# Optimization experiments

Measured on AMD Instinct MI355X. Metric: run time of the kernel, lower is better.

Reference implementation:

```python
import jax, jax.numpy as jnp
import numpy as np

D_MODEL = 1024
D_HEAD = 64
B, S = 4, 2048


def setup_inputs() -> dict:
    key = jax.random.key(0)
    ks = jax.random.split(key, 4)
    scale = 1.0 / np.sqrt(D_MODEL)
    return {
        "embeddings": jax.random.normal(ks[0], (B, S, D_MODEL), dtype=jnp.float32),
        "Wq": jax.random.normal(ks[1], (D_MODEL, D_HEAD), dtype=jnp.float32) * scale,
        "bq": jnp.zeros((D_HEAD,), dtype=jnp.float32),
        "Wk": jax.random.normal(ks[2], (D_MODEL, D_HEAD), dtype=jnp.float32) * scale,
        "bk": jnp.zeros((D_HEAD,), dtype=jnp.float32),
        "Wv": jax.random.normal(ks[3], (D_MODEL, D_HEAD), dtype=jnp.float32) * scale,
        "bv": jnp.zeros((D_HEAD,), dtype=jnp.float32),
    }


def reference(embeddings, Wq, bq, Wk, bk, Wv, bv):
    # Q, K, V projections: (b, s, d_head)
    Q = embeddings @ Wq + bq
    K = embeddings @ Wk + bk
    V = embeddings @ Wv + bv
    # scaled scores: (b, s, s)
    scores = jnp.einsum("bqd,bkd->bqk", Q, K) / jnp.sqrt(jnp.float32(D_HEAD))
    # causal mask: positions k > q get -inf
    s = scores.shape[-1]
    causal = jnp.tril(jnp.ones((s, s), dtype=bool))
    scores = jnp.where(causal, scores, -jnp.inf)
    pattern = jax.nn.softmax(scores, axis=-1)
    # attention output: (b, s, d_head)  (note: original forward skips self.output)
    return jnp.einsum("bqk,bkd->bqd", pattern, V)
```

## Files before the change

### kernel.cpp

```cpp
#include <hip/hip_runtime.h>
#include <hip/hip_bf16.h>

#define DMODEL 1024
#define DH 64
#define BB 4
#define SS 2048
#define NROW (BB * SS)
#define NS 8

typedef __attribute__((ext_vector_type(8))) short bf16x8;
typedef __attribute__((ext_vector_type(4))) float f32x4;

__device__ __forceinline__ unsigned short f2bf(float f) {
    __hip_bfloat16 h = __float2bfloat16(f);
    return __builtin_bit_cast(unsigned short, h);
}

__global__ __launch_bounds__(256) void prep_wt_kernel(
    const float* __restrict__ Wq, const float* __restrict__ Wk,
    const float* __restrict__ Wv, unsigned short* __restrict__ Wt)
{
    __shared__ float T[64][65];
    const int tid = threadIdx.x;
    const int m   = blockIdx.x;
    const int k0  = blockIdx.y * 64;
    const float* W = (m == 0) ? Wq : (m == 1) ? Wk : Wv;

    const int tn = tid & 63, tk = tid >> 6;
    #pragma unroll
    for (int j = 0; j < 16; ++j)
        T[4 * j + tk][tn] = W[(size_t)(k0 + 4 * j + tk) * DH + tn];
    __syncthreads();

    const int wk = tid & 63, wn = tid >> 6;
    #pragma unroll
    for (int j = 0; j < 16; ++j)
        Wt[(size_t)(m * 64 + 4 * j + wn) * DMODEL + k0 + wk] =
            f2bf(T[wk][4 * j + wn]);
}

__global__ __launch_bounds__(256) void qkv_proj_mfma(
    const float* __restrict__ emb, const unsigned short* __restrict__ Wt,
    const float* __restrict__ bq, const float* __restrict__ bk,
    const float* __restrict__ bv,
    unsigned short* __restrict__ Q, unsigned short* __restrict__ K,
    unsigned short* __restrict__ V)
{
    __shared__ unsigned short Bs[96 * 512];

    const int tid  = threadIdx.x;
    const int lane = tid & 63;
    const int w    = tid >> 6;
    const int c    = lane & 15;
    const int g    = lane >> 4;
    const int row0    = blockIdx.x * 64;
    const int colbase = blockIdx.y * 96;

    const float* arow = emb + (size_t)(row0 + 16 * w + c) * DMODEL + 8 * g;

    f32x4 acc[6];
    #pragma unroll
    for (int t = 0; t < 6; ++t) acc[t] = (f32x4){0.f, 0.f, 0.f, 0.f};

    float4 aR[4][4];

#define LOADA(KC, S, R) do {                                                  \
    aR[R][0] = *reinterpret_cast<const float4*>(arow + (KC)*512 + 64*(S));    \
    aR[R][1] = *reinterpret_cast<const float4*>(arow + (KC)*512 + 64*(S) + 4);\
    aR[R][2] = *reinterpret_cast<const float4*>(arow + (KC)*512 + 64*(S) + 32);\
    aR[R][3] = *reinterpret_cast<const float4*>(arow + (KC)*512 + 64*(S) + 36);\
} while (0)

    #pragma unroll
    for (int kc = 0; kc < 2; ++kc) {
        #pragma unroll
        for (int j = 0; j < 24; ++j) {
            const int r = 4 * j + w;
            __builtin_amdgcn_global_load_lds(
                (const __attribute__((address_space(1))) void*)(
                    Wt + (size_t)(colbase + r) * DMODEL + kc * 512
                       + 8 * (lane ^ (r & 7))),
                (__attribute__((address_space(3))) void*)&Bs[r * 512],
                16, 0, 0);
        }
        asm volatile("s_waitcnt vmcnt(0)" ::: "memory");
        __builtin_amdgcn_sched_barrier(0);
        __syncthreads();

        LOADA(kc, 0, 0);
        LOADA(kc, 1, 1);
        LOADA(kc, 2, 2);

        #pragma unroll
        for (int s = 0; s < 8; ++s) {
            const int r = s & 3;
            if (s + 3 < 8) LOADA(kc, s + 3, (s + 3) & 3);

            bf16x8 af[2];
            {
                union { bf16x8 v; unsigned short u[8]; } p0, p1;
                p0.u[0] = f2bf(aR[r][0].x); p0.u[1] = f2bf(aR[r][0].y);
                p0.u[2] = f2bf(aR[r][0].z); p0.u[3] = f2bf(aR[r][0].w);
                p0.u[4] = f2bf(aR[r][1].x); p0.u[5] = f2bf(aR[r][1].y);
                p0.u[6] = f2bf(aR[r][1].z); p0.u[7] = f2bf(aR[r][1].w);
                p1.u[0] = f2bf(aR[r][2].x); p1.u[1] = f2bf(aR[r][2].y);
                p1.u[2] = f2bf(aR[r][2].z); p1.u[3] = f2bf(aR[r][2].w);
                p1.u[4] = f2bf(aR[r][3].x); p1.u[5] = f2bf(aR[r][3].y);
                p1.u[6] = f2bf(aR[r][3].z); p1.u[7] = f2bf(aR[r][3].w);
                af[0] = p0.v; af[1] = p1.v;
            }

            #pragma unroll
            for (int t = 0; t < 6; ++t)
                #pragma unroll
                for (int kp = 0; kp < 2; ++kp) {
                    const int row  = 16 * t + c;
                    const int slot = (8 * s + 4 * kp + g) ^ (row & 7);
                    bf16x8 bfr = __builtin_bit_cast(bf16x8,
                        *reinterpret_cast<const uint4*>(&Bs[row * 512 + slot * 8]));
                    acc[t] = __builtin_amdgcn_mfma_f32_16x16x32_bf16(
                        af[kp], bfr, acc[t], 0, 0, 0);
                }
        }
        if (kc == 0) __syncthreads();
    }
#undef LOADA

    #pragma unroll
    for (int t = 0; t < 6; ++t) {
        const int col = colbase + 16 * t + c;
        const int m   = col >> 6;
        const int lc  = col & 63;
        const float* bias = (m == 0) ? bq : (m == 1) ? bk : bv;
        unsigned short* O = (m == 0) ? Q : (m == 1) ? K : V;
        const float bs    = bias[lc];
        const float scale = (m == 0) ? 0.125f : 1.0f;
        #pragma unroll
        for (int i = 0; i < 4; ++i) {
            const int rr = row0 + 16 * w + 4 * g + i;
            O[(size_t)rr * DH + lc] = f2bf((acc[t][i] + bs) * scale);
        }
    }
}

__global__ __launch_bounds__(256) void attn_mfma_split(
    const unsigned short* __restrict__ Q, const unsigned short* __restrict__ K,
    const unsigned short* __restrict__ V,
    float* __restrict__ Opart, float* __restrict__ mpart,
    float* __restrict__ lpart)
{
    __shared__ unsigned short Ks[64][72];
    __shared__ unsigned short Vt[64][72];
    __shared__ unsigned short Ps[4][16][72];

    const int tid  = threadIdx.x;
    const int lane = tid & 63;
    const int w    = tid >> 6;
    const int c    = lane & 15;
    const int g    = lane >> 4;
    const int qt   = blockIdx.x;
    const int b    = blockIdx.y;
    const int sp   = blockIdx.z;
    const int q0   = qt * 64;

    const int ntile = qt + 1;
    const int kt0 = (ntile * sp) / NS;
    const int kt1 = (ntile * (sp + 1)) / NS;

    const unsigned short* Qb = Q + (size_t)b * SS * DH;
    const unsigned short* Kb = K + (size_t)b * SS * DH;
    const unsigned short* Vb = V + (size_t)b * SS * DH;

    bf16x8 qa[2];
    #pragma unroll
    for (int kp = 0; kp < 2; ++kp)
        qa[kp] = __builtin_bit_cast(bf16x8,
            *reinterpret_cast<const uint4*>(
                &Qb[(size_t)(q0 + 16 * w + c) * DH + 32 * kp + 8 * g]));

    f32x4 o[4];
    #pragma unroll
    for (int t = 0; t < 4; ++t) o[t] = (f32x4){0.f, 0.f, 0.f, 0.f};
    float m_i = -1e30f;
    float l_i = 0.f;

    for (int kt = kt0; kt < kt1; ++kt) {
        const int kb0 = kt * 64;
        __syncthreads();
        #pragma unroll
        for (int j = 0; j < 2; ++j) {
            const int idx = tid + 256 * j;
            const int kv  = idx >> 3;
            const int m8  = idx & 7;
            const int d0  = m8 * 8;
            *reinterpret_cast<uint4*>(&Ks[kv][d0]) =
                *reinterpret_cast<const uint4*>(&Kb[(size_t)(kb0 + kv) * DH + d0]);
            const uint4 vv =
                *reinterpret_cast<const uint4*>(&Vb[(size_t)(kb0 + kv) * DH + d0]);
            const unsigned wd[4] = {vv.x, vv.y, vv.z, vv.w};
            #pragma unroll
            for (int e = 0; e < 8; ++e)
                Vt[(d0 + e) ^ m8][kv] =
                    (unsigned short)(wd[e >> 1] >> (16 * (e & 1)));
        }
        __syncthreads();

        f32x4 s[4];
        #pragma unroll
        for (int t = 0; t < 4; ++t) s[t] = (f32x4){0.f, 0.f, 0.f, 0.f};
        #pragma unroll
        for (int t = 0; t < 4; ++t)
            #pragma unroll
            for (int kp = 0; kp < 2; ++kp) {
                bf16x8 kf = __builtin_bit_cast(bf16x8,
                    *reinterpret_cast<const uint4*>(&Ks[16 * t + c][32 * kp + 8 * g]));
                s[t] = __builtin_amdgcn_mfma_f32_16x16x32_bf16(kf, qa[kp], s[t], 0, 0, 0);
            }

        if (kt == qt) {
            #pragma unroll
            for (int t = 0; t < 4; ++t)
                #pragma unroll
                for (int i = 0; i < 4; ++i)
                    if (16 * t + 4 * g + i > 16 * w + c) s[t][i] = -1e30f;
        }

        float mx = m_i;
        #pragma unroll
        for (int t = 0; t < 4; ++t)
            mx = fmaxf(mx, fmaxf(fmaxf(s[t][0], s[t][1]), fmaxf(s[t][2], s[t][3])));
        mx = fmaxf(mx, __shfl_xor(mx, 16));
        mx = fmaxf(mx, __shfl_xor(mx, 32));
        const float al = __expf(m_i - mx);
        m_i = mx;
        float sum = 0.f;
        #pragma unroll
        for (int t = 0; t < 4; ++t)
            #pragma unroll
            for (int i = 0; i < 4; ++i) {
                const float p = __expf(s[t][i] - mx);
                s[t][i] = p;
                sum += p;
            }
        sum += __shfl_xor(sum, 16);
        sum += __shfl_xor(sum, 32);
        l_i = l_i * al + sum;

        #pragma unroll
        for (int t = 0; t < 4; ++t) {
            uint2 u;
            u.x = (unsigned)f2bf(s[t][0]) | ((unsigned)f2bf(s[t][1]) << 16);
            u.y = (unsigned)f2bf(s[t][2]) | ((unsigned)f2bf(s[t][3]) << 16);
            *reinterpret_cast<uint2*>(&Ps[w][c][16 * t + 4 * g]) = u;
        }

        #pragma unroll
        for (int t = 0; t < 4; ++t)
            #pragma unroll
            for (int i = 0; i < 4; ++i)
                o[t][i] *= al;

        #pragma unroll
        for (int kp = 0; kp < 2; ++kp) {
            bf16x8 pb = __builtin_bit_cast(bf16x8,
                *reinterpret_cast<const uint4*>(&Ps[w][c][32 * kp + 8 * g]));
            #pragma unroll
            for (int t = 0; t < 4; ++t) {
                const int dv = 16 * t + c;
                const int pr = dv ^ ((2 * t + (c >> 3)) & 7);
                bf16x8 vf = __builtin_bit_cast(bf16x8,
                    *reinterpret_cast<const uint4*>(&Vt[pr][32 * kp + 8 * g]));
                o[t] = __builtin_amdgcn_mfma_f32_16x16x32_bf16(vf, pb, o[t], 0, 0, 0);
            }
        }
    }

    const int qrow = b * SS + q0 + 16 * w + c;
    #pragma unroll
    for (int t = 0; t < 4; ++t) {
        float4 v = {o[t][0], o[t][1], o[t][2], o[t][3]};
        *reinterpret_cast<float4*>(
            &Opart[((size_t)sp * NROW + qrow) * DH + 16 * t + 4 * g]) = v;
    }
    if (g == 0) {
        mpart[(size_t)sp * NROW + qrow] = m_i;
        lpart[(size_t)sp * NROW + qrow] = l_i;
    }
}

__global__ __launch_bounds__(256) void attn_combine(
    const float* __restrict__ Opart, const float* __restrict__ mpart,
    const float* __restrict__ lpart, float* __restrict__ out)
{
    const int idx = blockIdx.x * 256 + threadIdx.x;
    const int row = idx >> 4;
    const int d4  = (idx & 15) * 4;

    float m[NS];
    float M = -1e30f;
    #pragma unroll
    for (int s = 0; s < NS; ++s) {
        m[s] = mpart[(size_t)s * NROW + row];
        M = fmaxf(M, m[s]);
    }
    float L = 0.f;
    float4 acc = {0.f, 0.f, 0.f, 0.f};
    #pragma unroll
    for (int s = 0; s < NS; ++s) {
        const float wgt = __expf(m[s] - M);
        L += wgt * lpart[(size_t)s * NROW + row];
        const float4 p = *reinterpret_cast<const float4*>(
            &Opart[((size_t)s * NROW + row) * DH + d4]);
        acc.x += wgt * p.x; acc.y += wgt * p.y;
        acc.z += wgt * p.z; acc.w += wgt * p.w;
    }
    const float inv = 1.f / L;
    float4 r = {acc.x * inv, acc.y * inv, acc.z * inv, acc.w * inv};
    *reinterpret_cast<float4*>(&out[(size_t)row * DH + d4]) = r;
}

extern "C" void kernel_launch(void* const* d_in, const int* in_sizes, int n_in,
                              void* d_out, int out_size, void* d_ws, size_t ws_size,
                              hipStream_t stream) {
    const float* emb = (const float*)d_in[0];
    const float* Wq  = (const float*)d_in[1];
    const float* bq  = (const float*)d_in[2];
    const float* Wk  = (const float*)d_in[3];
    const float* bk  = (const float*)d_in[4];
    const float* Wv  = (const float*)d_in[5];
    const float* bv  = (const float*)d_in[6];
    float* out = (float*)d_out;

    unsigned short* Qw = (unsigned short*)d_ws;
    unsigned short* Kw = Qw + (size_t)NROW * DH;
    unsigned short* Vw = Kw + (size_t)NROW * DH;
    unsigned short* Wt = Vw + (size_t)NROW * DH;
    float* Opart = (float*)(Wt + (size_t)192 * DMODEL);
    float* mpart = Opart + (size_t)NS * NROW * DH;
    float* lpart = mpart + (size_t)NS * NROW;

    hipLaunchKernelGGL(prep_wt_kernel, dim3(3, 16), dim3(256), 0, stream,
                       Wq, Wk, Wv, Wt);
    hipLaunchKernelGGL(qkv_proj_mfma, dim3(NROW / 64, 2), dim3(256), 0, stream,
                       emb, Wt, bq, bk, bv, Qw, Kw, Vw);
    hipLaunchKernelGGL(attn_mfma_split, dim3(SS / 64, BB, NS), dim3(256), 0, stream,
                       Qw, Kw, Vw, Opart, mpart, lpart);
    hipLaunchKernelGGL(attn_combine, dim3(NROW * 16 / 256), dim3(256), 0, stream,
                       Opart, mpart, lpart, out);
}
```

Baseline: 49.47 us.

## Double-buffer weight tiles in QKV projection and store attention partials as bf16

The QKV projection kernel now splits the K dimension into four quarters and double-buffers the weight tiles in LDS. The next quarter's async global-to-LDS loads are issued while MFMAs run on the current one, instead of stalling on two large blocking loads. Separately, the split-attention partial outputs are written as bf16 rather than fp32, which halves the write and read traffic between the split kernel and the combine kernel. The cost is lower precision in the unnormalized partial sums and extra syncs per quarter.

New measurement: 44.90 us. -9.2%, faster.

```diff
diff --git a/kernel.cpp b/kernel.cpp
--- a/kernel.cpp
+++ b/kernel.cpp
@@ -14,6 +14,10 @@
 __device__ __forceinline__ unsigned short f2bf(float f) {
     __hip_bfloat16 h = __float2bfloat16(f);
     return __builtin_bit_cast(unsigned short, h);
+}
+__device__ __forceinline__ float bf2f(unsigned short u) {
+    unsigned v = (unsigned)u << 16;
+    return __builtin_bit_cast(float, v);
 }
 
 __global__ __launch_bounds__(256) void prep_wt_kernel(
@@ -46,7 +50,7 @@
     unsigned short* __restrict__ Q, unsigned short* __restrict__ K,
     unsigned short* __restrict__ V)
 {
-    __shared__ unsigned short Bs[96 * 512];
+    __shared__ unsigned short Bs[2][96][256];
 
     const int tid  = threadIdx.x;
     const int lane = tid & 63;
@@ -64,37 +68,48 @@
 
     float4 aR[4][4];
 
-#define LOADA(KC, S, R) do {                                                  \
-    aR[R][0] = *reinterpret_cast<const float4*>(arow + (KC)*512 + 64*(S));    \
-    aR[R][1] = *reinterpret_cast<const float4*>(arow + (KC)*512 + 64*(S) + 4);\
-    aR[R][2] = *reinterpret_cast<const float4*>(arow + (KC)*512 + 64*(S) + 32);\
-    aR[R][3] = *reinterpret_cast<const float4*>(arow + (KC)*512 + 64*(S) + 36);\
+    const int lrow_off = lane >> 5;
+    const int lslot    = lane & 31;
+
+#define ISSUEB(QTR, BI) do {                                                  \
+    _Pragma("unroll")                                                         \
+    for (int j = 0; j < 12; ++j) {                                            \
+        const int rb = 24 * w + 2 * j;                                        \
+        const int rr = rb + lrow_off;                                         \
+        __builtin_amdgcn_global_load_lds(                                     \
+            (const __attribute__((address_space(1))) void*)(                  \
+                Wt + (size_t)(colbase + rr) * DMODEL + (QTR) * 256            \
+                   + 8 * (lslot ^ (rr & 7))),                                 \
+            (__attribute__((address_space(3))) void*)&Bs[BI][rb][0],          \
+            16, 0, 0);                                                        \
+    }                                                                         \
 } while (0)
 
-    #pragma unroll
-    for (int kc = 0; kc < 2; ++kc) {
-        #pragma unroll
-        for (int j = 0; j < 24; ++j) {
-            const int r = 4 * j + w;
-            __builtin_amdgcn_global_load_lds(
-                (const __attribute__((address_space(1))) void*)(
-                    Wt + (size_t)(colbase + r) * DMODEL + kc * 512
-                       + 8 * (lane ^ (r & 7))),
-                (__attribute__((address_space(3))) void*)&Bs[r * 512],
-                16, 0, 0);
-        }
-        asm volatile("s_waitcnt vmcnt(0)" ::: "memory");
-        __builtin_amdgcn_sched_barrier(0);
-        __syncthreads();
-
-        LOADA(kc, 0, 0);
-        LOADA(kc, 1, 1);
-        LOADA(kc, 2, 2);
-
-        #pragma unroll
-        for (int s = 0; s < 8; ++s) {
-            const int r = s & 3;
-            if (s + 3 < 8) LOADA(kc, s + 3, (s + 3) & 3);
+#define LOADA(S, R) do {                                                      \
+    aR[R][0] = *reinterpret_cast<const float4*>(arow + 64 * (S));             \
+    aR[R][1] = *reinterpret_cast<const float4*>(arow + 64 * (S) + 4);         \
+    aR[R][2] = *reinterpret_cast<const float4*>(arow + 64 * (S) + 32);        \
+    aR[R][3] = *reinterpret_cast<const float4*>(arow + 64 * (S) + 36);        \
+} while (0)
+
+    ISSUEB(0, 0);
+    LOADA(0, 0);
+    LOADA(1, 1);
+    LOADA(2, 2);
+    asm volatile("s_waitcnt vmcnt(0)" ::: "memory");
+    __builtin_amdgcn_sched_barrier(0);
+    __syncthreads();
+
+    #pragma unroll
+    for (int q = 0; q < 4; ++q) {
+        const int bi = q & 1;
+        if (q < 3) ISSUEB(q + 1, bi ^ 1);
+
+        #pragma unroll
+        for (int s2 = 0; s2 < 4; ++s2) {
+            const int S = 4 * q + s2;
+            const int r = S & 3;
+            if (S + 3 < 16) LOADA(S + 3, (S + 3) & 3);
 
             bf16x8 af[2];
             {
@@ -115,15 +130,20 @@
                 #pragma unroll
                 for (int kp = 0; kp < 2; ++kp) {
                     const int row  = 16 * t + c;
-                    const int slot = (8 * s + 4 * kp + g) ^ (row & 7);
+                    const int slot = (8 * s2 + 4 * kp + g) ^ (row & 7);
                     bf16x8 bfr = __builtin_bit_cast(bf16x8,
-                        *reinterpret_cast<const uint4*>(&Bs[row * 512 + slot * 8]));
+                        *reinterpret_cast<const uint4*>(&Bs[bi][row][slot * 8]));
                     acc[t] = __builtin_amdgcn_mfma_f32_16x16x32_bf16(
                         af[kp], bfr, acc[t], 0, 0, 0);
                 }
         }
-        if (kc == 0) __syncthreads();
-    }
+        if (q < 3) {
+            asm volatile("s_waitcnt vmcnt(0)" ::: "memory");
+            __builtin_amdgcn_sched_barrier(0);
+            __syncthreads();
+        }
+    }
+#undef ISSUEB
 #undef LOADA
 
     #pragma unroll
@@ -146,7 +166,7 @@
 __global__ __launch_bounds__(256) void attn_mfma_split(
     const unsigned short* __restrict__ Q, const unsigned short* __restrict__ K,
     const unsigned short* __restrict__ V,
-    float* __restrict__ Opart, float* __restrict__ mpart,
+    unsigned short* __restrict__ Opart, float* __restrict__ mpart,
     float* __restrict__ lpart)
 {
     __shared__ unsigned short Ks[64][72];
@@ -278,9 +298,11 @@
     const int qrow = b * SS + q0 + 16 * w + c;
     #pragma unroll
     for (int t = 0; t < 4; ++t) {
-        float4 v = {o[t][0], o[t][1], o[t][2], o[t][3]};
-        *reinterpret_cast<float4*>(
-            &Opart[((size_t)sp * NROW + qrow) * DH + 16 * t + 4 * g]) = v;
+        uint2 u;
+        u.x = (unsigned)f2bf(o[t][0]) | ((unsigned)f2bf(o[t][1]) << 16);
+        u.y = (unsigned)f2bf(o[t][2]) | ((unsigned)f2bf(o[t][3]) << 16);
+        *reinterpret_cast<uint2*>(
+            &Opart[((size_t)sp * NROW + qrow) * DH + 16 * t + 4 * g]) = u;
     }
     if (g == 0) {
         mpart[(size_t)sp * NROW + qrow] = m_i;
@@ -289,7 +311,7 @@
 }
 
 __global__ __launch_bounds__(256) void attn_combine(
-    const float* __restrict__ Opart, const float* __restrict__ mpart,
+    const unsigned short* __restrict__ Opart, const float* __restrict__ mpart,
     const float* __restrict__ lpart, float* __restrict__ out)
 {
     const int idx = blockIdx.x * 256 + threadIdx.x;
@@ -309,10 +331,12 @@
     for (int s = 0; s < NS; ++s) {
         const float wgt = __expf(m[s] - M);
         L += wgt * lpart[(size_t)s * NROW + row];
-        const float4 p = *reinterpret_cast<const float4*>(
+        const uint2 pu = *reinterpret_cast<const uint2*>(
             &Opart[((size_t)s * NROW + row) * DH + d4]);
-        acc.x += wgt * p.x; acc.y += wgt * p.y;
-        acc.z += wgt * p.z; acc.w += wgt * p.w;
+        acc.x += wgt * bf2f((unsigned short)(pu.x & 0xffff));
+        acc.y += wgt * bf2f((unsigned short)(pu.x >> 16));
+        acc.z += wgt * bf2f((unsigned short)(pu.y & 0xffff));
+        acc.w += wgt * bf2f((unsigned short)(pu.y >> 16));
     }
     const float inv = 1.f / L;
     float4 r = {acc.x * inv, acc.y * inv, acc.z * inv, acc.w * inv};
@@ -335,8 +359,8 @@
     unsigned short* Kw = Qw + (size_t)NROW * DH;
     unsigned short* Vw = Kw + (size_t)NROW * DH;
     unsigned short* Wt = Vw + (size_t)NROW * DH;
-    float* Opart = (float*)(Wt + (size_t)192 * DMODEL);
-    float* mpart = Opart + (size_t)NS * NROW * DH;
+    unsigned short* Opart = Wt + (size_t)192 * DMODEL;
+    float* mpart = (float*)(Opart + (size_t)NS * NROW * DH);
     float* lpart = mpart + (size_t)NS * NROW;
 
     hipLaunchKernelGGL(prep_wt_kernel, dim3(3, 16), dim3(256), 0, stream,
```
